# Performance work log

Measured on AMD Instinct MI355X. Metric: run time of the kernel, lower is better.

The kernel has to match this reference:

```python
import jax, jax.numpy as jnp
import numpy as np

S = 2048          # total tokens (prefill, batch folded into seq dim)
H = 32            # num query heads
HKV = 8           # num kv heads (GQA)
G = H // HKV      # query heads per kv head
D = 128           # head_dim
SCALE = D ** -0.5 # flex_attention default scale
DIFF_BS = 32      # diffusion block size for the block mask


def setup_inputs() -> dict:
    key = jax.random.key(0)
    k1, k2, k3 = jax.random.split(key, 3)
    q = jax.random.normal(k1, (S, H * D), dtype=jnp.float32)
    k = jax.random.normal(k2, (S, HKV * D), dtype=jnp.float32)
    v = jax.random.normal(k3, (S, HKV * D), dtype=jnp.float32)
    # diffusion block-causal mask: token i attends to all tokens in diffusion
    # blocks up to and including its own block (matches attn_metadata.block_mask
    # semantics fed into dllm_block_mask / flex_attention)
    blk = jnp.arange(S) // DIFF_BS
    block_mask = blk[:, None] >= blk[None, :]  # [S, S] bool
    return {"q": q, "k": k, "v": v, "block_mask": block_mask}


def reference(q, k, v, block_mask):
    # q: [S, H*D]; k, v: [S, HKV*D]; block_mask: [S, S] bool
    qh = q.reshape(S, HKV, G, D)   # group query heads by shared kv head (enable_gqa)
    kh = k.reshape(S, HKV, D)
    vh = v.reshape(S, HKV, D)
    # scores: [HKV, G, S_q, S_k]
    scores = jnp.einsum('qhgd,khd->hgqk', qh, kh) * SCALE
    neg = jnp.finfo(scores.dtype).min
    scores = jnp.where(block_mask[None, None, :, :], scores, neg)
    p = jax.nn.softmax(scores, axis=-1)
    o = jnp.einsum('hgqk,khd->qhgd', p, vh)  # [S, HKV, G, D]
    # prefill epilogue: rearrange '1 h s d -> s (h d)'
    return o.reshape(S, H * D)
```

## Files before the change

### kernel.cpp

```cpp
#include <hip/hip_runtime.h>
#include <hip/hip_bf16.h>

typedef __attribute__((ext_vector_type(8)))  short short8;
typedef __attribute__((ext_vector_type(16))) float f32x16;
typedef unsigned short u16;
typedef unsigned int   u32;

__device__ __forceinline__ u16 f2b(float f){
    __hip_bfloat16 h = __float2bfloat16(f);
    u16 u; __builtin_memcpy(&u, &h, 2); return u;
}
__device__ __forceinline__ u32 pk2(float lo, float hi){
    return (u32)f2b(lo) | ((u32)f2b(hi) << 16);
}
__device__ __forceinline__ float b2f(u16 u){
    u32 w = ((u32)u) << 16; float f; __builtin_memcpy(&f, &w, 4); return f;
}

#define PART_STRIDE 8448

template<bool SPLIT>
__global__ __launch_bounds__(512, 2)
void dllm_attn(const float* __restrict__ Qg, const float* __restrict__ Kg,
               const float* __restrict__ Vg, float* __restrict__ Og,
               char* __restrict__ Wg)
{
    __shared__ alignas(16) char kl[64 * 256];
    __shared__ alignas(16) char vl[128 * 128];

    const int bid = blockIdx.x;
    const int kh  = bid & 7;
    int tq2, ci, uu = 0;
    if (SPLIT){
        uu = 79 - (bid >> 3);
        if (uu < 8)       { tq2 = uu; ci = 0; }
        else if (uu < 24) { const int x = uu - 8;  tq2 = 8  + (x >> 1); ci = x & 1; }
        else if (uu < 48) { const int x = uu - 24; const int d3 = x / 3; tq2 = 16 + d3; ci = x - 3 * d3; }
        else              { const int x = uu - 48; tq2 = 24 + (x >> 2); ci = x & 3; }
    } else { tq2 = 31 - (bid >> 3); ci = 0; }
    const int ntt = tq2 + 1;
    const int t0  = SPLIT ? (ci << 3) : 0;
    const int t1  = SPLIT ? min(t0 + 8, ntt) : ntt;
    const int nch = SPLIT ? ((tq2 >> 3) + 1) : 1;

    const int tid = threadIdx.x;
    const int wv  = tid >> 6;
    const int ln  = tid & 63;
    const int lq  = ln & 31;
    const int hi  = ln >> 5;
    const int swz = (lq & 7) << 4;
    const int hgrp = wv & 3;
    const int half = wv >> 2;
    const int h   = (kh << 2) + hgrp;
    const int qw0 = (tq2 << 6) + (half << 5);
    const int nvis = qw0 + 32;

    const float QS = 0.088388347648318447f * 1.4426950408889634f;
    short8 qf[8];
    {
        const float* qp = Qg + (size_t)(qw0 + lq) * 4096 + h * 128 + hi * 8;
        #pragma unroll
        for (int ds = 0; ds < 8; ++ds){
            const float4 a = *reinterpret_cast<const float4*>(qp + ds * 16);
            const float4 b = *reinterpret_cast<const float4*>(qp + ds * 16 + 4);
            qf[ds] = __builtin_bit_cast(short8,
                make_uint4(pk2(a.x * QS, a.y * QS), pk2(a.z * QS, a.w * QS),
                           pk2(b.x * QS, b.y * QS), pk2(b.z * QS, b.w * QS)));
        }
    }

    f32x16 oa[4];
    #pragma unroll
    for (int i = 0; i < 4; ++i)
        #pragma unroll
        for (int j = 0; j < 16; ++j) oa[i][j] = 0.f;
    float mR = -1e30f, lR = 0.f;

    const int krow = tid >> 3;
    const int kdc  = tid & 7;
    const int vk0  = wv << 3;
    const int dA   = ln;

    for (int t = t0; t < t1; ++t){
        const int kv0 = t << 6;
        const bool full = (kv0 + 64) <= nvis;

        __syncthreads();
        {
            const float* kp = Kg + (size_t)(kv0 + krow) * 1024 + (kh << 7) + (kdc << 4);
            const float4 a = *reinterpret_cast<const float4*>(kp);
            const float4 b = *reinterpret_cast<const float4*>(kp + 4);
            const float4 c = *reinterpret_cast<const float4*>(kp + 8);
            const float4 d = *reinterpret_cast<const float4*>(kp + 12);
            const int kb = krow * 256 + (kdc << 5);
            const int key = (krow & 7) << 4;
            *reinterpret_cast<uint4*>(&kl[krow * 256 + ((kdc << 5) ^ key)]) =
                make_uint4(pk2(a.x,a.y), pk2(a.z,a.w), pk2(b.x,b.y), pk2(b.z,b.w));
            *reinterpret_cast<uint4*>(&kl[krow * 256 + (((kdc << 5) + 16) ^ key)]) =
                make_uint4(pk2(c.x,c.y), pk2(c.z,c.w), pk2(d.x,d.y), pk2(d.z,d.w));
            (void)kb;
            const float* vp = Vg + (size_t)(kv0 + vk0) * 1024 + (kh << 7);
            float va[8], vb[8];
            #pragma unroll
            for (int j = 0; j < 8; ++j){
                va[j] = vp[j * 1024 + dA];
                vb[j] = vp[j * 1024 + 64 + dA];
            }
            *reinterpret_cast<uint4*>(&vl[dA * 128 + ((vk0 << 1) ^ ((dA & 7) << 4))]) =
                make_uint4(pk2(va[0],va[1]), pk2(va[2],va[3]),
                           pk2(va[4],va[5]), pk2(va[6],va[7]));
            const int dB = dA + 64;
            *reinterpret_cast<uint4*>(&vl[dB * 128 + ((vk0 << 1) ^ ((dB & 7) << 4))]) =
                make_uint4(pk2(vb[0],vb[1]), pk2(vb[2],vb[3]),
                           pk2(vb[4],vb[5]), pk2(vb[6],vb[7]));
        }
        __syncthreads();

        f32x16 s0, s1;
        #pragma unroll
        for (int i = 0; i < 16; ++i){ s0[i] = 0.f; s1[i] = 0.f; }
        __builtin_amdgcn_s_setprio(1);
        #pragma unroll
        for (int ds = 0; ds < 8; ++ds){
            const short8 a0 = *reinterpret_cast<const short8*>(
                &kl[lq * 256 + (((ds << 5) + (hi << 4)) ^ swz)]);
            s0 = __builtin_amdgcn_mfma_f32_32x32x16_bf16(a0, qf[ds], s0, 0, 0, 0);
        }
        if (full){
            #pragma unroll
            for (int ds = 0; ds < 8; ++ds){
                const short8 a1 = *reinterpret_cast<const short8*>(
                    &kl[(32 + lq) * 256 + (((ds << 5) + (hi << 4)) ^ swz)]);
                s1 = __builtin_amdgcn_mfma_f32_32x32x16_bf16(a1, qf[ds], s1, 0, 0, 0);
            }
        }
        __builtin_amdgcn_s_setprio(0);

        float p0[16], p1[16];
        float mx = -1e30f;
        #pragma unroll
        for (int r = 0; r < 16; ++r){ p0[r] = s0[r]; mx = fmaxf(mx, s0[r]); }
        if (full){
            #pragma unroll
            for (int r = 0; r < 16; ++r){ p1[r] = s1[r]; mx = fmaxf(mx, s1[r]); }
        }
        mx = fmaxf(mx, __shfl_xor(mx, 32, 64));
        const float mn = fmaxf(mR, mx);
        const float cf = __builtin_exp2f(mR - mn);
        mR = mn;
        float ps = 0.f;
        #pragma unroll
        for (int r = 0; r < 16; ++r){ p0[r] = __builtin_exp2f(p0[r] - mn); ps += p0[r]; }
        if (full){
            #pragma unroll
            for (int r = 0; r < 16; ++r){ p1[r] = __builtin_exp2f(p1[r] - mn); ps += p1[r]; }
        }
        ps += __shfl_xor(ps, 32, 64);
        lR = lR * cf + ps;
        #pragma unroll
        for (int i = 0; i < 4; ++i)
            #pragma unroll
            for (int j = 0; j < 16; ++j) oa[i][j] *= cf;

        u32 pw0[8], px0[8], pw1[8], px1[8];
        #pragma unroll
        for (int rr = 0; rr < 8; ++rr){
            pw0[rr] = pk2(p0[2*rr], p0[2*rr+1]);
            px0[rr] = (u32)__shfl_xor((int)pw0[rr], 32, 64);
        }
        if (full){
            #pragma unroll
            for (int rr = 0; rr < 8; ++rr){
                pw1[rr] = pk2(p1[2*rr], p1[2*rr+1]);
                px1[rr] = (u32)__shfl_xor((int)pw1[rr], 32, 64);
            }
        }

        short8 pf[4];
        #pragma unroll
        for (int ks = 0; ks < 4; ++ks){
            if (ks < 2 || full){
                const u32* pwt = (ks >> 1) ? pw1 : pw0;
                const u32* pxt = (ks >> 1) ? px1 : px0;
                u32 wb[4];
                #pragma unroll
                for (int w = 0; w < 4; ++w){
                    const int b = (w & 1) + ((ks & 1) << 2);
                    const u32 own = hi ? pwt[b + 2] : pwt[b];
                    const u32 oth = hi ? pxt[b + 2] : pxt[b];
                    wb[w] = (hi == (w >> 1)) ? own : oth;
                }
                pf[ks] = __builtin_bit_cast(short8, make_uint4(wb[0], wb[1], wb[2], wb[3]));
            }
        }

        __builtin_amdgcn_s_setprio(1);
        #pragma unroll
        for (int dt = 0; dt < 4; ++dt){
            #pragma unroll
            for (int ks = 0; ks < 4; ++ks){
                if (ks < 2 || full){
                    const short8 vf = *reinterpret_cast<const short8*>(
                        &vl[((dt << 5) + lq) * 128 + (((ks << 5) + (hi << 4)) ^ swz)]);
                    oa[dt] = __builtin_amdgcn_mfma_f32_32x32x16_bf16(vf, pf[ks], oa[dt], 0, 0, 0);
                }
            }
        }
        __builtin_amdgcn_s_setprio(0);
    }

    if (!SPLIT || nch == 1){
        const float rl = 1.f / lR;
        float* op = Og + (size_t)(qw0 + lq) * 4096 + (h << 7) + (hi << 2);
        #pragma unroll
        for (int dt = 0; dt < 4; ++dt){
            #pragma unroll
            for (int g2 = 0; g2 < 4; ++g2){
                float4 w4;
                w4.x = oa[dt][4*g2 + 0] * rl;
                w4.y = oa[dt][4*g2 + 1] * rl;
                w4.z = oa[dt][4*g2 + 2] * rl;
                w4.w = oa[dt][4*g2 + 3] * rl;
                *reinterpret_cast<float4*>(op + (dt << 5) + (g2 << 3)) = w4;
            }
        }
    } else {
        const int pu = ((kh * 72 + (uu - 8)) << 3) + wv;
        char* base = Wg + (size_t)pu * PART_STRIDE;
        #pragma unroll
        for (int i = 0; i < 8; ++i){
            const int e0 = i * 8;
            uint4 w4;
            w4.x = pk2(oa[(e0+0)>>4][(e0+0)&15], oa[(e0+1)>>4][(e0+1)&15]);
            w4.y = pk2(oa[(e0+2)>>4][(e0+2)&15], oa[(e0+3)>>4][(e0+3)&15]);
            w4.z = pk2(oa[(e0+4)>>4][(e0+4)&15], oa[(e0+5)>>4][(e0+5)&15]);
            w4.w = pk2(oa[(e0+6)>>4][(e0+6)&15], oa[(e0+7)>>4][(e0+7)&15]);
            *reinterpret_cast<uint4*>(base + ln * 128 + i * 16) = w4;
        }
        if (hi == 0){
            *reinterpret_cast<float*>(base + 8192 + lq * 4) = mR;
            *reinterpret_cast<float*>(base + 8320 + lq * 4) = lR;
        }
    }
}

__global__ __launch_bounds__(256, 2)
void dllm_merge(float* __restrict__ Og, const char* __restrict__ Wg)
{
    const int b    = blockIdx.x;
    const int h    = b & 31;
    const int r    = b >> 5;
    const int tq2  = 8 + (r >> 1);
    const int half = r & 1;
    const int kh = h >> 2, hgrp = h & 3;
    const int wvIdx = (half << 2) | hgrp;
    const int nch = (tq2 >> 3) + 1;
    int cb;
    if (tq2 < 16)      cb = (tq2 - 8) << 1;
    else if (tq2 < 24) cb = 16 + (tq2 - 16) * 3;
    else               cb = 40 + ((tq2 - 24) << 2);

    const int tid = threadIdx.x;
    const int q   = tid >> 3;
    const int s   = tid & 7;

    const char* bases[4];
    float mv[4], lv[4];
    float M = -1e30f;
    #pragma unroll
    for (int c = 0; c < 4; ++c){
        if (c < nch){
            bases[c] = Wg + (size_t)(((kh * 72 + cb + c) << 3) + wvIdx) * PART_STRIDE;
            mv[c] = *reinterpret_cast<const float*>(bases[c] + 8192 + q * 4);
            lv[c] = *reinterpret_cast<const float*>(bases[c] + 8320 + q * 4);
            M = fmaxf(M, mv[c]);
        }
    }
    uint4 wlo[4], whi[4];
    #pragma unroll
    for (int c = 0; c < 4; ++c){
        if (c < nch){
            wlo[c] = *reinterpret_cast<const uint4*>(bases[c] + q * 128 + s * 16);
            whi[c] = *reinterpret_cast<const uint4*>(bases[c] + (q + 32) * 128 + s * 16);
        }
    }
    float wsum = 0.f;
    float acc[16];
    #pragma unroll
    for (int e = 0; e < 16; ++e) acc[e] = 0.f;
    #pragma unroll
    for (int c = 0; c < 4; ++c){
        if (c < nch){
            const float w = __builtin_exp2f(mv[c] - M);
            wsum += lv[c] * w;
            const u32 wl[4] = {wlo[c].x, wlo[c].y, wlo[c].z, wlo[c].w};
            const u32 wh[4] = {whi[c].x, whi[c].y, whi[c].z, whi[c].w};
            #pragma unroll
            for (int k = 0; k < 4; ++k){
                const int dl = ((k & 1) << 1) + ((k >> 1) << 3);
                acc[dl + 0] += b2f((u16)(wl[k] & 0xffffu)) * w;
                acc[dl + 1] += b2f((u16)(wl[k] >> 16)) * w;
                acc[dl + 4] += b2f((u16)(wh[k] & 0xffffu)) * w;
                acc[dl + 5] += b2f((u16)(wh[k] >> 16)) * w;
            }
        }
    }
    const float rl = 1.f / wsum;
    float* op = Og + (size_t)((tq2 << 6) + (half << 5) + q) * 4096 + h * 128 + (s << 4);
    #pragma unroll
    for (int g = 0; g < 4; ++g){
        float4 v4;
        v4.x = acc[g*4 + 0] * rl;
        v4.y = acc[g*4 + 1] * rl;
        v4.z = acc[g*4 + 2] * rl;
        v4.w = acc[g*4 + 3] * rl;
        *reinterpret_cast<float4*>(op + (g << 2)) = v4;
    }
}

extern "C" void kernel_launch(void* const* d_in, const int* in_sizes, int n_in,
                              void* d_out, int out_size, void* d_ws, size_t ws_size,
                              hipStream_t stream) {
    const float* Q = (const float*)d_in[0];
    const float* K = (const float*)d_in[1];
    const float* V = (const float*)d_in[2];
    float* O = (float*)d_out;
    const size_t need = (size_t)4608 * PART_STRIDE;
    if (ws_size >= need){
        dllm_attn<true><<<dim3(640), dim3(512), 0, stream>>>(Q, K, V, O, (char*)d_ws);
        dllm_merge<<<dim3(1536), dim3(256), 0, stream>>>(O, (const char*)d_ws);
    } else {
        dllm_attn<false><<<dim3(256), dim3(512), 0, stream>>>(Q, K, V, O, (char*)d_ws);
    }
}
```

Before: 211.5 us.

## Double-buffer K/V tiles, refine KV split to 4-tile chunks, lazy softmax rescale

Adds register prefetch of the next K/V tile with double-buffered LDS, which drops one barrier per iteration and overlaps global loads with MFMA work. The split-KV decomposition is generalized to a chunk size CT, and CT=4 is used when the workspace allows, so more blocks are launched and the merge handles up to 8 partials. The online softmax skips rescaling the accumulator while the row max grows by no more than 8 (log2 units), saving VALU work. In exchange, LDS use doubles, launch_bounds now requests 4 blocks per CU, and merge traffic grows with the extra partials.

```diff
diff --git a/kernel.cpp b/kernel.cpp
--- a/kernel.cpp
+++ b/kernel.cpp
@@ -19,29 +19,34 @@
 
 #define PART_STRIDE 8448
 
-template<bool SPLIT>
-__global__ __launch_bounds__(512, 2)
+template<int CT, bool SPLIT>
+__global__ __launch_bounds__(512, 4)
 void dllm_attn(const float* __restrict__ Qg, const float* __restrict__ Kg,
                const float* __restrict__ Vg, float* __restrict__ Og,
                char* __restrict__ Wg)
 {
-    __shared__ alignas(16) char kl[64 * 256];
-    __shared__ alignas(16) char vl[128 * 128];
-
+    __shared__ alignas(16) char kl[2 * 64 * 256];
+    __shared__ alignas(16) char vl[2 * 128 * 128];
+
+    const int RECS = (CT == 4) ? 140 : 72;
     const int bid = blockIdx.x;
     const int kh  = bid & 7;
     int tq2, ci, uu = 0;
     if (SPLIT){
-        uu = 79 - (bid >> 3);
-        if (uu < 8)       { tq2 = uu; ci = 0; }
-        else if (uu < 24) { const int x = uu - 8;  tq2 = 8  + (x >> 1); ci = x & 1; }
-        else if (uu < 48) { const int x = uu - 24; const int d3 = x / 3; tq2 = 16 + d3; ci = x - 3 * d3; }
-        else              { const int x = uu - 48; tq2 = 24 + (x >> 2); ci = x & 3; }
+        const int NU = (CT == 4) ? 144 : 80;
+        uu = (NU - 1) - (bid >> 3);
+        int g = 0;
+        #pragma unroll
+        for (int gg = 1; gg < 8; ++gg)
+            if ((CT * gg * (gg + 1)) / 2 <= uu) g = gg;
+        const int rem = uu - (CT * g * (g + 1)) / 2;
+        tq2 = CT * g + rem / (g + 1);
+        ci  = rem % (g + 1);
     } else { tq2 = 31 - (bid >> 3); ci = 0; }
     const int ntt = tq2 + 1;
-    const int t0  = SPLIT ? (ci << 3) : 0;
-    const int t1  = SPLIT ? min(t0 + 8, ntt) : ntt;
-    const int nch = SPLIT ? ((tq2 >> 3) + 1) : 1;
+    const int t0  = SPLIT ? (ci * CT) : 0;
+    const int t1  = SPLIT ? min(t0 + CT, ntt) : ntt;
+    const int nch = SPLIT ? (tq2 / CT + 1) : 1;
 
     const int tid = threadIdx.x;
     const int wv  = tid >> 6;
@@ -78,44 +83,67 @@
 
     const int krow = tid >> 3;
     const int kdc  = tid & 7;
+    const int kkey = (krow & 7) << 4;
     const int vk0  = wv << 3;
     const int dA   = ln;
-
+    const int vkey = (dA & 7) << 4;
+
+    u32 kpk[8], vpk[8];
+    {
+        const int kv0 = t0 << 6;
+        const float* kp = Kg + (size_t)(kv0 + krow) * 1024 + (kh << 7) + (kdc << 4);
+        const float4 a = *reinterpret_cast<const float4*>(kp);
+        const float4 b = *reinterpret_cast<const float4*>(kp + 4);
+        const float4 c = *reinterpret_cast<const float4*>(kp + 8);
+        const float4 d = *reinterpret_cast<const float4*>(kp + 12);
+        kpk[0]=pk2(a.x,a.y); kpk[1]=pk2(a.z,a.w); kpk[2]=pk2(b.x,b.y); kpk[3]=pk2(b.z,b.w);
+        kpk[4]=pk2(c.x,c.y); kpk[5]=pk2(c.z,c.w); kpk[6]=pk2(d.x,d.y); kpk[7]=pk2(d.z,d.w);
+        const float* vp = Vg + (size_t)(kv0 + vk0) * 1024 + (kh << 7);
+        float va[8], vb[8];
+        #pragma unroll
+        for (int j = 0; j < 8; ++j){ va[j] = vp[j*1024 + dA]; vb[j] = vp[j*1024 + 64 + dA]; }
+        vpk[0]=pk2(va[0],va[1]); vpk[1]=pk2(va[2],va[3]); vpk[2]=pk2(va[4],va[5]); vpk[3]=pk2(va[6],va[7]);
+        vpk[4]=pk2(vb[0],vb[1]); vpk[5]=pk2(vb[2],vb[3]); vpk[6]=pk2(vb[4],vb[5]); vpk[7]=pk2(vb[6],vb[7]);
+    }
+
+    int buf = 0;
     for (int t = t0; t < t1; ++t){
         const int kv0 = t << 6;
         const bool full = (kv0 + 64) <= nvis;
 
+        {
+            const int kb = (buf << 14) + krow * 256;
+            *reinterpret_cast<uint4*>(&kl[kb + ((kdc << 5) ^ kkey)]) =
+                make_uint4(kpk[0], kpk[1], kpk[2], kpk[3]);
+            *reinterpret_cast<uint4*>(&kl[kb + (((kdc << 5) + 16) ^ kkey)]) =
+                make_uint4(kpk[4], kpk[5], kpk[6], kpk[7]);
+            const int vb0 = (buf << 14);
+            *reinterpret_cast<uint4*>(&vl[vb0 + dA * 128 + ((vk0 << 1) ^ vkey)]) =
+                make_uint4(vpk[0], vpk[1], vpk[2], vpk[3]);
+            *reinterpret_cast<uint4*>(&vl[vb0 + (dA + 64) * 128 + ((vk0 << 1) ^ vkey)]) =
+                make_uint4(vpk[4], vpk[5], vpk[6], vpk[7]);
+        }
         __syncthreads();
+
         {
-            const float* kp = Kg + (size_t)(kv0 + krow) * 1024 + (kh << 7) + (kdc << 4);
+            const int tn  = min(t + 1, t1 - 1);
+            const int kvn = tn << 6;
+            const float* kp = Kg + (size_t)(kvn + krow) * 1024 + (kh << 7) + (kdc << 4);
             const float4 a = *reinterpret_cast<const float4*>(kp);
             const float4 b = *reinterpret_cast<const float4*>(kp + 4);
             const float4 c = *reinterpret_cast<const float4*>(kp + 8);
             const float4 d = *reinterpret_cast<const float4*>(kp + 12);
-            const int kb = krow * 256 + (kdc << 5);
-            const int key = (krow & 7) << 4;
-            *reinterpret_cast<uint4*>(&kl[krow * 256 + ((kdc << 5) ^ key)]) =
-                make_uint4(pk2(a.x,a.y), pk2(a.z,a.w), pk2(b.x,b.y), pk2(b.z,b.w));
-            *reinterpret_cast<uint4*>(&kl[krow * 256 + (((kdc << 5) + 16) ^ key)]) =
-                make_uint4(pk2(c.x,c.y), pk2(c.z,c.w), pk2(d.x,d.y), pk2(d.z,d.w));
-            (void)kb;
-            const float* vp = Vg + (size_t)(kv0 + vk0) * 1024 + (kh << 7);
+            const float* vp = Vg + (size_t)(kvn + vk0) * 1024 + (kh << 7);
             float va[8], vb[8];
             #pragma unroll
-            for (int j = 0; j < 8; ++j){
-                va[j] = vp[j * 1024 + dA];
-                vb[j] = vp[j * 1024 + 64 + dA];
-            }
-            *reinterpret_cast<uint4*>(&vl[dA * 128 + ((vk0 << 1) ^ ((dA & 7) << 4))]) =
-                make_uint4(pk2(va[0],va[1]), pk2(va[2],va[3]),
-                           pk2(va[4],va[5]), pk2(va[6],va[7]));
-            const int dB = dA + 64;
-            *reinterpret_cast<uint4*>(&vl[dB * 128 + ((vk0 << 1) ^ ((dB & 7) << 4))]) =
-                make_uint4(pk2(vb[0],vb[1]), pk2(vb[2],vb[3]),
-                           pk2(vb[4],vb[5]), pk2(vb[6],vb[7]));
-        }
-        __syncthreads();
-
+            for (int j = 0; j < 8; ++j){ va[j] = vp[j*1024 + dA]; vb[j] = vp[j*1024 + 64 + dA]; }
+            kpk[0]=pk2(a.x,a.y); kpk[1]=pk2(a.z,a.w); kpk[2]=pk2(b.x,b.y); kpk[3]=pk2(b.z,b.w);
+            kpk[4]=pk2(c.x,c.y); kpk[5]=pk2(c.z,c.w); kpk[6]=pk2(d.x,d.y); kpk[7]=pk2(d.z,d.w);
+            vpk[0]=pk2(va[0],va[1]); vpk[1]=pk2(va[2],va[3]); vpk[2]=pk2(va[4],va[5]); vpk[3]=pk2(va[6],va[7]);
+            vpk[4]=pk2(vb[0],vb[1]); vpk[5]=pk2(vb[2],vb[3]); vpk[6]=pk2(vb[4],vb[5]); vpk[7]=pk2(vb[6],vb[7]);
+        }
+
+        const int kb0 = buf << 14;
         f32x16 s0, s1;
         #pragma unroll
         for (int i = 0; i < 16; ++i){ s0[i] = 0.f; s1[i] = 0.f; }
@@ -123,14 +151,14 @@
         #pragma unroll
         for (int ds = 0; ds < 8; ++ds){
             const short8 a0 = *reinterpret_cast<const short8*>(
-                &kl[lq * 256 + (((ds << 5) + (hi << 4)) ^ swz)]);
+                &kl[kb0 + lq * 256 + (((ds << 5) + (hi << 4)) ^ swz)]);
             s0 = __builtin_amdgcn_mfma_f32_32x32x16_bf16(a0, qf[ds], s0, 0, 0, 0);
         }
         if (full){
             #pragma unroll
             for (int ds = 0; ds < 8; ++ds){
                 const short8 a1 = *reinterpret_cast<const short8*>(
-                    &kl[(32 + lq) * 256 + (((ds << 5) + (hi << 4)) ^ swz)]);
+                    &kl[kb0 + (32 + lq) * 256 + (((ds << 5) + (hi << 4)) ^ swz)]);
                 s1 = __builtin_amdgcn_mfma_f32_32x32x16_bf16(a1, qf[ds], s1, 0, 0, 0);
             }
         }
@@ -145,9 +173,18 @@
             for (int r = 0; r < 16; ++r){ p1[r] = s1[r]; mx = fmaxf(mx, s1[r]); }
         }
         mx = fmaxf(mx, __shfl_xor(mx, 32, 64));
-        const float mn = fmaxf(mR, mx);
-        const float cf = __builtin_exp2f(mR - mn);
-        mR = mn;
+        float mn = fmaxf(mR, mx);
+        if (__all(mx - mR <= 8.0f)){
+            mn = mR;
+        } else {
+            const float cf = __builtin_exp2f(mR - mn);
+            lR *= cf;
+            #pragma unroll
+            for (int i = 0; i < 4; ++i)
+                #pragma unroll
+                for (int j = 0; j < 16; ++j) oa[i][j] *= cf;
+            mR = mn;
+        }
         float ps = 0.f;
         #pragma unroll
         for (int r = 0; r < 16; ++r){ p0[r] = __builtin_exp2f(p0[r] - mn); ps += p0[r]; }
@@ -156,11 +193,7 @@
             for (int r = 0; r < 16; ++r){ p1[r] = __builtin_exp2f(p1[r] - mn); ps += p1[r]; }
         }
         ps += __shfl_xor(ps, 32, 64);
-        lR = lR * cf + ps;
-        #pragma unroll
-        for (int i = 0; i < 4; ++i)
-            #pragma unroll
-            for (int j = 0; j < 16; ++j) oa[i][j] *= cf;
+        lR += ps;
 
         u32 pw0[8], px0[8], pw1[8], px1[8];
         #pragma unroll
@@ -201,12 +234,13 @@
             for (int ks = 0; ks < 4; ++ks){
                 if (ks < 2 || full){
                     const short8 vf = *reinterpret_cast<const short8*>(
-                        &vl[((dt << 5) + lq) * 128 + (((ks << 5) + (hi << 4)) ^ swz)]);
+                        &vl[kb0 + ((dt << 5) + lq) * 128 + (((ks << 5) + (hi << 4)) ^ swz)]);
                     oa[dt] = __builtin_amdgcn_mfma_f32_32x32x16_bf16(vf, pf[ks], oa[dt], 0, 0, 0);
                 }
             }
         }
         __builtin_amdgcn_s_setprio(0);
+        buf ^= 1;
     }
 
     if (!SPLIT || nch == 1){
@@ -225,7 +259,7 @@
             }
         }
     } else {
-        const int pu = ((kh * 72 + (uu - 8)) << 3) + wv;
+        const int pu = ((kh * RECS + (uu - CT)) << 3) + wv;
         char* base = Wg + (size_t)pu * PART_STRIDE;
         #pragma unroll
         for (int i = 0; i < 8; ++i){
@@ -244,42 +278,43 @@
     }
 }
 
+template<int CT>
 __global__ __launch_bounds__(256, 2)
 void dllm_merge(float* __restrict__ Og, const char* __restrict__ Wg)
 {
+    const int RECS = (CT == 4) ? 140 : 72;
+    const int MAXC = (CT == 4) ? 8 : 4;
     const int b    = blockIdx.x;
     const int h    = b & 31;
     const int r    = b >> 5;
-    const int tq2  = 8 + (r >> 1);
+    const int tq2  = CT + (r >> 1);
     const int half = r & 1;
     const int kh = h >> 2, hgrp = h & 3;
     const int wvIdx = (half << 2) | hgrp;
-    const int nch = (tq2 >> 3) + 1;
-    int cb;
-    if (tq2 < 16)      cb = (tq2 - 8) << 1;
-    else if (tq2 < 24) cb = 16 + (tq2 - 16) * 3;
-    else               cb = 40 + ((tq2 - 24) << 2);
+    const int g   = tq2 / CT;
+    const int nch = g + 1;
+    const int uu0 = (CT * g * (g + 1)) / 2 + (tq2 - CT * g) * (g + 1);
 
     const int tid = threadIdx.x;
     const int q   = tid >> 3;
     const int s   = tid & 7;
 
-    const char* bases[4];
-    float mv[4], lv[4];
+    const char* bases[8];
+    float mv[8], lv[8];
     float M = -1e30f;
     #pragma unroll
-    for (int c = 0; c < 4; ++c){
-        if (c < nch){
-            bases[c] = Wg + (size_t)(((kh * 72 + cb + c) << 3) + wvIdx) * PART_STRIDE;
+    for (int c = 0; c < 8; ++c){
+        if (c < MAXC && c < nch){
+            bases[c] = Wg + (size_t)(((kh * RECS + uu0 - CT + c) << 3) + wvIdx) * PART_STRIDE;
             mv[c] = *reinterpret_cast<const float*>(bases[c] + 8192 + q * 4);
             lv[c] = *reinterpret_cast<const float*>(bases[c] + 8320 + q * 4);
             M = fmaxf(M, mv[c]);
         }
     }
-    uint4 wlo[4], whi[4];
-    #pragma unroll
-    for (int c = 0; c < 4; ++c){
-        if (c < nch){
+    uint4 wlo[8], whi[8];
+    #pragma unroll
+    for (int c = 0; c < 8; ++c){
+        if (c < MAXC && c < nch){
             wlo[c] = *reinterpret_cast<const uint4*>(bases[c] + q * 128 + s * 16);
             whi[c] = *reinterpret_cast<const uint4*>(bases[c] + (q + 32) * 128 + s * 16);
         }
@@ -289,8 +324,8 @@
     #pragma unroll
     for (int e = 0; e < 16; ++e) acc[e] = 0.f;
     #pragma unroll
-    for (int c = 0; c < 4; ++c){
-        if (c < nch){
+    for (int c = 0; c < 8; ++c){
+        if (c < MAXC && c < nch){
             const float w = __builtin_exp2f(mv[c] - M);
             wsum += lv[c] * w;
             const u32 wl[4] = {wlo[c].x, wlo[c].y, wlo[c].z, wlo[c].w};
@@ -308,13 +343,13 @@
     const float rl = 1.f / wsum;
     float* op = Og + (size_t)((tq2 << 6) + (half << 5) + q) * 4096 + h * 128 + (s << 4);
     #pragma unroll
-    for (int g = 0; g < 4; ++g){
+    for (int gg = 0; gg < 4; ++gg){
         float4 v4;
-        v4.x = acc[g*4 + 0] * rl;
-        v4.y = acc[g*4 + 1] * rl;
-        v4.z = acc[g*4 + 2] * rl;
-        v4.w = acc[g*4 + 3] * rl;
-        *reinterpret_cast<float4*>(op + (g << 2)) = v4;
+        v4.x = acc[gg*4 + 0] * rl;
+        v4.y = acc[gg*4 + 1] * rl;
+        v4.z = acc[gg*4 + 2] * rl;
+        v4.w = acc[gg*4 + 3] * rl;
+        *reinterpret_cast<float4*>(op + (gg << 2)) = v4;
     }
 }
 
@@ -325,11 +360,15 @@
     const float* K = (const float*)d_in[1];
     const float* V = (const float*)d_in[2];
     float* O = (float*)d_out;
-    const size_t need = (size_t)4608 * PART_STRIDE;
-    if (ws_size >= need){
-        dllm_attn<true><<<dim3(640), dim3(512), 0, stream>>>(Q, K, V, O, (char*)d_ws);
-        dllm_merge<<<dim3(1536), dim3(256), 0, stream>>>(O, (const char*)d_ws);
+    const size_t need4 = (size_t)8 * 140 * 8 * PART_STRIDE;
+    const size_t need8 = (size_t)8 *  72 * 8 * PART_STRIDE;
+    if (ws_size >= need4){
+        dllm_attn<4, true><<<dim3(1152), dim3(512), 0, stream>>>(Q, K, V, O, (char*)d_ws);
+        dllm_merge<4><<<dim3(1792), dim3(256), 0, stream>>>(O, (const char*)d_ws);
+    } else if (ws_size >= need8){
+        dllm_attn<8, true><<<dim3(640), dim3(512), 0, stream>>>(Q, K, V, O, (char*)d_ws);
+        dllm_merge<8><<<dim3(1536), dim3(256), 0, stream>>>(O, (const char*)d_ws);
     } else {
-        dllm_attn<false><<<dim3(256), dim3(512), 0, stream>>>(Q, K, V, O, (char*)d_ws);
-    }
-}
+        dllm_attn<4, false><<<dim3(256), dim3(512), 0, stream>>>(Q, K, V, O, (char*)d_ws);
+    }
+}
```

After: 644.8 us. 205% more time.
